# Kernel optimization log

Hardware: AMD Instinct MI355X
Metric: run time of the kernel (lower is better)

Reference implementation:

```python
import jax, jax.numpy as jnp
import numpy as np

N_XI = 512      # internal REN state dim
L = 128         # nonlinearity channels (sequential loop length)
N_STATES = 128  # plant state dim (w)
N_INPUTS = 64   # control input dim (u)
EPS = 0.001
STD = 0.1
BATCH = 32768


def _model_params(X, Y):
    """set_model_param(): derive constrained REN matrices from free params X, Y."""
    n, l = N_XI, L
    H = X.T @ X + EPS * jnp.eye(2 * n + l, dtype=X.dtype)
    H11 = H[:n, :n]
    H21 = H[n:n + l, :n]
    H22 = H[n:n + l, n:n + l]
    H31 = H[n + l:, :n]
    H32 = H[n + l:, n:n + l]
    H33 = H[n + l:, n + l:]
    Fm = H31                                 # (n_xi, n_xi)
    B1 = H32                                 # (n_xi, l)
    E = 0.5 * (H11 + H33 + Y - Y.T)          # (n_xi, n_xi)
    Lam = 0.5 * jnp.diag(H22)                # (l,) strictly positive
    D11 = -jnp.tril(H22, -1)                 # strictly lower triangular (l, l)
    C1 = -H21                                # (l, n_xi)
    return Fm, B1, E, Lam, D11, C1


def setup_inputs() -> dict:
    key = jax.random.key(0)
    ks = jax.random.split(key, 9)
    n, l = N_XI, L
    return {
        "t": 0,
        "w": jax.random.normal(ks[0], (BATCH, 1, N_STATES), jnp.float32),
        "xi": jax.random.normal(ks[1], (BATCH, 1, n), jnp.float32),
        "X": jax.random.normal(ks[2], (2 * n + l, 2 * n + l), jnp.float32) * STD,
        "Y": jax.random.normal(ks[3], (n, n), jnp.float32) * STD,
        "B2": jax.random.normal(ks[4], (n, N_STATES), jnp.float32) * STD,
        "C2": jax.random.normal(ks[5], (N_INPUTS, n), jnp.float32) * STD,
        "D21": jax.random.normal(ks[6], (N_INPUTS, l), jnp.float32) * STD,
        "D22": jax.random.normal(ks[7], (N_INPUTS, N_STATES), jnp.float32) * STD,
        "D12": jax.random.normal(ks[8], (l, N_STATES), jnp.float32) * STD,
    }


def reference(t, w, xi, X, Y, B2, C2, D21, D22, D12):
    Fm, B1, E, Lam, D11, C1 = _model_params(X, Y)
    w2 = w[:, 0, :]    # (B, num_states)
    xi2 = xi[:, 0, :]  # (B, n_xi)

    # Precompute the xi- and w-dependent parts of every row's pre-activation.
    pre = xi2 @ C1.T + w2 @ D12.T  # (B, l)

    eye = jnp.eye(L, dtype=pre.dtype)

    def step(eps, xs):
        # Sequential forward substitution: row i only reads eps[:, :i]
        # because D11 is strictly lower triangular.
        d_row, p_col, lam, e_row = xs
        v = p_col + eps @ d_row            # (B,)
        e = jnp.tanh(v / lam)
        return eps + e[:, None] * e_row[None, :], None

    eps0 = jnp.zeros_like(pre)
    epsilon, _ = jax.lax.scan(step, eps0, (D11, pre.T, Lam, eye))  # (B, l)

    E_xi = xi2 @ Fm.T + epsilon @ B1.T + w2 @ B2.T      # (B, n_xi)
    xi_ = E_xi @ jnp.linalg.inv(E).T                    # (B, n_xi)
    u = xi2 @ C2.T + epsilon @ D21.T + w2 @ D22.T       # (B, num_inputs)
    return u[:, None, :], xi_[:, None, :]
```

## Files before the change

kernel.cpp:

```cpp
#include <hip/hip_runtime.h>
#include <cstddef>

#define NXI   512
#define LL    128
#define NST   128
#define NU    64
#define BATCH 32768
#define TW    1152
#define EPSC  0.001f
#define KC    768
#define NC    576
#define NCP   640

typedef unsigned short u16;
typedef __attribute__((ext_vector_type(8))) short   short8;
typedef __attribute__((ext_vector_type(4))) short   short4v;
typedef __attribute__((ext_vector_type(4))) float   f32x4;

__device__ __forceinline__ u16 f2bf(float f) {
    unsigned u = __float_as_uint(f);
    u += 0x7FFFu + ((u >> 16) & 1u);
    return (u16)(u >> 16);
}

__global__ __launch_bounds__(256) void k_transpose(const float* __restrict__ X, u16* __restrict__ XT) {
    __shared__ float t[32][33];
    int tx = threadIdx.x & 31, ty = threadIdx.x >> 5;
    int bx = blockIdx.x, by = blockIdx.y;
    #pragma unroll
    for (int q = 0; q < 4; q++) {
        int r = ty + q * 8;
        t[r][tx] = X[(size_t)(by * 32 + r) * TW + bx * 32 + tx];
    }
    __syncthreads();
    #pragma unroll
    for (int q = 0; q < 4; q++) {
        int r = ty + q * 8;
        XT[(size_t)(bx * 32 + r) * TW + by * 32 + tx] = f2bf(t[tx][r]);
    }
}

__global__ __launch_bounds__(256) void k_build_Ac(const float* __restrict__ xi, const float* __restrict__ w,
                                                  u16* __restrict__ Ac) {
    size_t t = (size_t)blockIdx.x * 256 + threadIdx.x;
    int b = (int)(t / 80), ch = (int)(t % 80);
    const float* src;
    int col;
    if (ch < 64) { src = xi + (size_t)b * NXI + ch * 8;        col = ch * 8; }
    else         { src = w  + (size_t)b * NST + (ch - 64) * 8; col = 640 + (ch - 64) * 8; }
    f32x4 a = ((const f32x4*)src)[0], c = ((const f32x4*)src)[1];
    short8 o;
    o[0]=(short)f2bf(a[0]); o[1]=(short)f2bf(a[1]); o[2]=(short)f2bf(a[2]); o[3]=(short)f2bf(a[3]);
    o[4]=(short)f2bf(c[0]); o[5]=(short)f2bf(c[1]); o[6]=(short)f2bf(c[2]); o[7]=(short)f2bf(c[3]);
    *(short8*)(Ac + (size_t)b * KC + col) = o;
}

__global__ __launch_bounds__(256) void k_gemm2(const u16* __restrict__ A, int lda,
                                               const u16* __restrict__ W, int ldw,
                                               float* __restrict__ C0, int ldc0, int nsplit,
                                               float* __restrict__ C1, int ldc1,
                                               int K, int nbx, int ntrue, int swz) {
    __shared__ __align__(16) u16 As[128 * 32];
    __shared__ __align__(16) u16 Bs[128 * 32];
    int id = blockIdx.x;
    int bx, by;
    if (swz) {
        int j = id >> 3;
        int per = (int)(gridDim.x >> 3) / nbx;
        by = (id & 7) * per + j / nbx;
        bx = j - (j / nbx) * nbx;
    } else {
        by = id / nbx;
        bx = id - by * nbx;
    }
    const int tid = threadIdx.x;
    const int wave = tid >> 6, lane = tid & 63, quad = lane >> 4, l16 = lane & 15;
    const int bm0 = by * 128, bn0 = bx * 128;
    const int srow = tid >> 2, sch = (tid & 3) * 8;
    const u16* ga0 = A + (size_t)(bm0 + srow) * lda + sch;
    const u16* ga1 = ga0 + (size_t)64 * lda;
    const u16* gb0 = W + (size_t)(bn0 + srow) * ldw + sch;
    const u16* gb1 = gb0 + (size_t)64 * ldw;
    u16* la = As + wave * 512;
    u16* lb = Bs + wave * 512;
    const int mb = (wave >> 1) * 64, nb = (wave & 1) * 64;

    f32x4 acc[4][4];
    #pragma unroll
    for (int i = 0; i < 4; i++)
        #pragma unroll
        for (int j = 0; j < 4; j++) acc[i][j] = (f32x4){0.f, 0.f, 0.f, 0.f};

    for (int kt = 0; kt < K; kt += 32) {
        __syncthreads();
        __builtin_amdgcn_global_load_lds((void*)(ga0 + kt), (void*)la,          16, 0, 0);
        __builtin_amdgcn_global_load_lds((void*)(ga1 + kt), (void*)(la + 2048), 16, 0, 0);
        __builtin_amdgcn_global_load_lds((void*)(gb0 + kt), (void*)lb,          16, 0, 0);
        __builtin_amdgcn_global_load_lds((void*)(gb1 + kt), (void*)(lb + 2048), 16, 0, 0);
        __syncthreads();
        short8 af[4], bf[4];
        #pragma unroll
        for (int mt = 0; mt < 4; mt++) af[mt] = *(const short8*)&As[(mb + mt * 16 + l16) * 32 + quad * 8];
        #pragma unroll
        for (int nt = 0; nt < 4; nt++) bf[nt] = *(const short8*)&Bs[(nb + nt * 16 + l16) * 32 + quad * 8];
        #pragma unroll
        for (int mt = 0; mt < 4; mt++)
            #pragma unroll
            for (int nt = 0; nt < 4; nt++)
                acc[mt][nt] = __builtin_amdgcn_mfma_f32_16x16x32_bf16(af[mt], bf[nt], acc[mt][nt], 0, 0, 0);
    }
    #pragma unroll
    for (int mt = 0; mt < 4; mt++)
        #pragma unroll
        for (int nt = 0; nt < 4; nt++)
            #pragma unroll
            for (int r = 0; r < 4; r++) {
                int row = bm0 + mb + mt * 16 + quad * 4 + r;
                int col = bn0 + nb + nt * 16 + l16;
                if (col < ntrue) {
                    float v = acc[mt][nt][r];
                    if (col < nsplit) C0[(size_t)row * ldc0 + col] = v;
                    else              C1[(size_t)row * ldc1 + (col - nsplit)] = v;
                }
            }
}

__global__ __launch_bounds__(256) void k_derive(const float* __restrict__ Hm, const float* __restrict__ Y,
                                                const float* __restrict__ B2, const float* __restrict__ D12,
                                                float* __restrict__ Agj, float* __restrict__ D11,
                                                float* __restrict__ rlam, u16* __restrict__ W1) {
    int idx = blockIdx.x * 256 + threadIdx.x;
    const int n0 = 512 * 1280, n1 = 128 * 128, n2 = 128, n3 = 128 * KC;
    if (idx < n0) {
        int i = idx / 1280, j = idx % 1280;
        float val;
        if (j < 512) {
            val = 0.5f * (Hm[(size_t)i * TW + j] + Hm[(size_t)(640 + i) * TW + 640 + j]
                          + Y[(size_t)i * 512 + j] - Y[(size_t)j * 512 + i]);
            if (i == j) val += EPSC;
        } else if (j < 1024) {
            val = Hm[(size_t)(640 + i) * TW + (j - 512)];
        } else if (j < 1152) {
            val = Hm[(size_t)(640 + i) * TW + 512 + (j - 1024)];
        } else {
            val = B2[(size_t)i * NST + (j - 1152)];
        }
        Agj[idx] = val;
        return;
    }
    idx -= n0;
    if (idx < n1) {
        int i = idx >> 7, j = idx & 127;
        D11[idx] = (j < i) ? -Hm[(size_t)(512 + i) * TW + 512 + j] : 0.f;
        return;
    }
    idx -= n1;
    if (idx < n2) {
        rlam[idx] = 2.0f / (Hm[(size_t)(512 + idx) * TW + 512 + idx] + EPSC);
        return;
    }
    idx -= n2;
    if (idx < n3) {
        int i = idx / KC, c = idx % KC;
        float v;
        if (c < 512)      v = -Hm[(size_t)(512 + i) * TW + c];
        else if (c < 640) v = 0.f;
        else              v = D12[(size_t)i * NST + (c - 640)];
        W1[(size_t)i * KC + c] = f2bf(v);
    }
}

__device__ __forceinline__ void invert64(float* Cl, float* Sa, float* Sb, float* mcol,
                                         float* rp, float* __restrict__ invOut, int tid) {
    int r = tid >> 2, c = tid & 3;
    float a[16], b[16];
    #pragma unroll
    for (int q = 0; q < 4; q++) {
        f32x4 v = *(f32x4*)&Cl[r * 68 + c * 16 + q * 4];
        a[q*4+0]=v[0]; a[q*4+1]=v[1]; a[q*4+2]=v[2]; a[q*4+3]=v[3];
    }
    #pragma unroll
    for (int j = 0; j < 16; j++) b[j] = (c * 16 + j == r) ? 1.f : 0.f;

    #pragma unroll
    for (int k = 0; k < 64; k++) {
        const int kc = k >> 4, kl = k & 15;
        if (r == k) {
            #pragma unroll
            for (int q = 0; q < 4; q++) {
                *(f32x4*)&Sa[c * 16 + q * 4] = (f32x4){a[q*4], a[q*4+1], a[q*4+2], a[q*4+3]};
                *(f32x4*)&Sb[c * 16 + q * 4] = (f32x4){b[q*4], b[q*4+1], b[q*4+2], b[q*4+3]};
            }
        }
        if (c == kc) {
            mcol[r] = a[kl];
            if (r == k) rp[0] = 1.0f / a[kl];
        }
        __syncthreads();
        float m = (mcol[r] - ((r == k) ? 1.0f : 0.0f)) * rp[0];
        #pragma unroll
        for (int q = 0; q < 4; q++) {
            f32x4 sa = *(f32x4*)&Sa[c * 16 + q * 4];
            f32x4 sb = *(f32x4*)&Sb[c * 16 + q * 4];
            a[q*4+0] = fmaf(-m, sa[0], a[q*4+0]); a[q*4+1] = fmaf(-m, sa[1], a[q*4+1]);
            a[q*4+2] = fmaf(-m, sa[2], a[q*4+2]); a[q*4+3] = fmaf(-m, sa[3], a[q*4+3]);
            b[q*4+0] = fmaf(-m, sb[0], b[q*4+0]); b[q*4+1] = fmaf(-m, sb[1], b[q*4+1]);
            b[q*4+2] = fmaf(-m, sb[2], b[q*4+2]); b[q*4+3] = fmaf(-m, sb[3], b[q*4+3]);
        }
        __syncthreads();
    }
    #pragma unroll
    for (int q = 0; q < 4; q++)
        *(f32x4*)&invOut[r * 64 + c * 16 + q * 4] = (f32x4){b[q*4], b[q*4+1], b[q*4+2], b[q*4+3]};
}

__global__ __launch_bounds__(256) void k_diaginv0(const float* __restrict__ Agj, float* __restrict__ invD) {
    __shared__ __align__(16) float Cl[64 * 68];
    __shared__ float Sa[64], Sb[64], mcol[64], rp[1];
    int tid = threadIdx.x, r = tid >> 2, c4 = tid & 3;
    #pragma unroll
    for (int q = 0; q < 4; q++)
        *(f32x4*)&Cl[r * 68 + c4 * 16 + q * 4] = *(const f32x4*)(Agj + (size_t)r * 1280 + c4 * 16 + q * 4);
    __syncthreads();
    invert64(Cl, Sa, Sb, mcol, rp, invD, tid);
}

__global__ __launch_bounds__(256) void k_elim(float* __restrict__ Agj, float* __restrict__ invD, int k) {
    __shared__ __align__(16) float invDs[64 * 68];
    __shared__ __align__(16) float Ps[64 * 68];
    __shared__ __align__(16) float Ss[64 * 68];
    __shared__ __align__(16) float Ms[64 * 68];
    __shared__ float Sa[64], Sb[64], mcol[64], rp[1];
    int tid = threadIdx.x;
    int by = blockIdx.y, bx = blockIdx.x;
    int rb = by + (by >= k ? 1 : 0);
    int cb = k + 1 + bx;
    int lr = tid >> 2, lc = tid & 3;
    #pragma unroll
    for (int q = 0; q < 4; q++) {
        *(f32x4*)&invDs[lr * 68 + lc * 16 + q * 4] = *(const f32x4*)(invD + (size_t)k * 4096 + lr * 64 + lc * 16 + q * 4);
        *(f32x4*)&Ps[lr * 68 + lc * 16 + q * 4]    = *(const f32x4*)(Agj + (size_t)(k * 64 + lr) * 1280 + cb * 64 + lc * 16 + q * 4);
        *(f32x4*)&Ms[lr * 68 + lc * 16 + q * 4]    = *(const f32x4*)(Agj + (size_t)(rb * 64 + lr) * 1280 + k * 64 + lc * 16 + q * 4);
    }
    __syncthreads();
    int ty = tid >> 4, tx = tid & 15;
    f32x4 s[4];
    #pragma unroll
    for (int ri = 0; ri < 4; ri++) s[ri] = (f32x4){0.f, 0.f, 0.f, 0.f};
    for (int kk = 0; kk < 64; kk++) {
        f32x4 pv = *(f32x4*)&Ps[kk * 68 + tx * 4];
        #pragma unroll
        for (int ri = 0; ri < 4; ri++) s[ri] += pv * invDs[(ty * 4 + ri) * 68 + kk];
    }
    #pragma unroll
    for (int ri = 0; ri < 4; ri++) *(f32x4*)&Ss[(ty * 4 + ri) * 68 + tx * 4] = s[ri];
    __syncthreads();
    f32x4 accv[4];
    #pragma unroll
    for (int ri = 0; ri < 4; ri++)
        accv[ri] = *(const f32x4*)(Agj + (size_t)(rb * 64 + ty * 4 + ri) * 1280 + cb * 64 + tx * 4);
    for (int kk = 0; kk < 64; kk++) {
        f32x4 sv = *(f32x4*)&Ss[kk * 68 + tx * 4];
        #pragma unroll
        for (int ri = 0; ri < 4; ri++) accv[ri] -= sv * Ms[(ty * 4 + ri) * 68 + kk];
    }
    #pragma unroll
    for (int ri = 0; ri < 4; ri++)
        *(f32x4*)(Agj + (size_t)(rb * 64 + ty * 4 + ri) * 1280 + cb * 64 + tx * 4) = accv[ri];
    if (k < 7 && bx == 0 && by == k) {
        __syncthreads();
        #pragma unroll
        for (int ri = 0; ri < 4; ri++) *(f32x4*)&Ps[(ty * 4 + ri) * 68 + tx * 4] = accv[ri];
        __syncthreads();
        invert64(Ps, Sa, Sb, mcol, rp, invD + (size_t)(k + 1) * 4096, tid);
    }
}

__global__ __launch_bounds__(256) void k_finalize(const float* __restrict__ Agj, const float* __restrict__ invD,
                                                  const float* __restrict__ C2, const float* __restrict__ D21,
                                                  const float* __restrict__ D22, u16* __restrict__ Wc) {
    __shared__ __align__(16) float invDs[64 * 68];
    __shared__ __align__(16) float Ps[64 * 68];
    int tid = threadIdx.x, bx = blockIdx.x, by = blockIdx.y;
    int ty = tid >> 4, tx = tid & 15;
    if (by >= 8) {
        #pragma unroll
        for (int ri = 0; ri < 4; ri++) {
            int q = ty * 4 + ri;
            int row = 512 + (by - 8) * 64 + q;
            int cbase = bx * 64 + tx * 4;
            short4v o;
            if (by == 8) {
                f32x4 v;
                if (cbase < 512)      v = *(const f32x4*)(C2 + (size_t)q * 512 + cbase);
                else if (cbase < 640) v = *(const f32x4*)(D21 + (size_t)q * NST + (cbase - 512));
                else                  v = *(const f32x4*)(D22 + (size_t)q * NST + (cbase - 640));
                o[0]=(short)f2bf(v[0]); o[1]=(short)f2bf(v[1]); o[2]=(short)f2bf(v[2]); o[3]=(short)f2bf(v[3]);
            } else {
                o[0]=0; o[1]=0; o[2]=0; o[3]=0;
            }
            *(short4v*)(Wc + (size_t)row * KC + cbase) = o;
        }
        return;
    }
    int lr = tid >> 2, lc = tid & 3;
    #pragma unroll
    for (int q = 0; q < 4; q++) {
        *(f32x4*)&invDs[lr * 68 + lc * 16 + q * 4] = *(const f32x4*)(invD + (size_t)by * 4096 + lr * 64 + lc * 16 + q * 4);
        *(f32x4*)&Ps[lr * 68 + lc * 16 + q * 4]    = *(const f32x4*)(Agj + (size_t)(by * 64 + lr) * 1280 + 512 + bx * 64 + lc * 16 + q * 4);
    }
    __syncthreads();
    f32x4 s[4];
    #pragma unroll
    for (int ri = 0; ri < 4; ri++) s[ri] = (f32x4){0.f, 0.f, 0.f, 0.f};
    for (int kk = 0; kk < 64; kk++) {
        f32x4 pv = *(f32x4*)&Ps[kk * 68 + tx * 4];
        #pragma unroll
        for (int ri = 0; ri < 4; ri++) s[ri] += pv * invDs[(ty * 4 + ri) * 68 + kk];
    }
    #pragma unroll
    for (int ri = 0; ri < 4; ri++) {
        short4v o; o[0]=(short)f2bf(s[ri][0]); o[1]=(short)f2bf(s[ri][1]); o[2]=(short)f2bf(s[ri][2]); o[3]=(short)f2bf(s[ri][3]);
        *(short4v*)(Wc + (size_t)(by * 64 + ty * 4 + ri) * KC + bx * 64 + tx * 4) = o;
    }
}

__global__ __launch_bounds__(1024) void k_scan(const float* __restrict__ pre, const float* __restrict__ D11,
                                               const float* __restrict__ rlam, u16* __restrict__ Ac) {
    __shared__ __align__(16) float D11s[128 * 132];
    int tid = threadIdx.x;
    {
        int r = tid >> 3, c = (tid & 7) * 16;
        const f32x4* src = (const f32x4*)(D11 + (size_t)r * 128 + c);
        f32x4 v0 = src[0], v1 = src[1], v2 = src[2], v3 = src[3];
        f32x4* dst = (f32x4*)&D11s[r * 132 + c];
        dst[0] = v0; dst[1] = v1; dst[2] = v2; dst[3] = v3;
    }
    int lg = tid & 15;
    int row = blockIdx.x * 64 + (tid >> 4);
    int gbase = (tid & 63) & ~15;
    const float L2E2 = 2.885390082f;

    float corrv[8], a8[8];
    #pragma unroll
    for (int b = 0; b < 8; b++) {
        corrv[b] = pre[(size_t)row * 128 + b * 16 + lg];
        a8[b] = L2E2 * rlam[b * 16 + lg];
    }
    __syncthreads();

    #pragma unroll
    for (int b = 0; b < 8; b++) {
        f32x4 dblk[4];
        #pragma unroll
        for (int q = 0; q < 4; q++)
            dblk[q] = *(const f32x4*)&D11s[(b * 16 + lg) * 132 + b * 16 + q * 4];
        float v = corrv[b];
        float a = a8[b];
        float e16[16];
        float myeps = 0.f;
        #pragma unroll
        for (int t = 0; t < 16; t++) {
            float ex = __builtin_amdgcn_exp2f(a * v);
            float cand = 1.0f - 2.0f * __builtin_amdgcn_rcpf(ex + 1.0f);
            float e = __shfl(cand, gbase + t, 64);
            e16[t] = e;
            if (lg == t) myeps = e;
            v = fmaf(e, dblk[t >> 2][t & 3], v);
        }
        Ac[(size_t)row * KC + 512 + b * 16 + lg] = f2bf(myeps);
        #pragma unroll
        for (int bb = b + 1; bb < 8; bb++) {
            f32x4 dd[4];
            #pragma unroll
            for (int q = 0; q < 4; q++)
                dd[q] = *(const f32x4*)&D11s[(bb * 16 + lg) * 132 + b * 16 + q * 4];
            float acc = corrv[bb];
            #pragma unroll
            for (int t = 0; t < 16; t++)
                acc = fmaf(e16[t], dd[t >> 2][t & 3], acc);
            corrv[bb] = acc;
        }
    }
}

extern "C" void kernel_launch(void* const* d_in, const int* in_sizes, int n_in,
                              void* d_out, int out_size, void* d_ws, size_t ws_size,
                              hipStream_t stream) {
    const float* w_in  = (const float*)d_in[1];
    const float* xi_in = (const float*)d_in[2];
    const float* X   = (const float*)d_in[3];
    const float* Y   = (const float*)d_in[4];
    const float* B2  = (const float*)d_in[5];
    const float* C2  = (const float*)d_in[6];
    const float* D21 = (const float*)d_in[7];
    const float* D22 = (const float*)d_in[8];
    const float* D12 = (const float*)d_in[9];
    float* out_u  = (float*)d_out;
    float* out_xi = (float*)d_out + (size_t)BATCH * NU;

    char* base = (char*)d_ws;
    size_t off = 0;
    auto carve = [&](size_t bytes) -> void* {
        void* p = base + off;
        off += (bytes + 255) & ~(size_t)255;
        return p;
    };
    u16*   XT   = (u16*)  carve((size_t)TW * TW * 2);
    u16*   Ac   = (u16*)  carve((size_t)BATCH * KC * 2);
    float* Hm   = (float*)carve((size_t)TW * TW * 4);
    float* Agj  = (float*)carve((size_t)512 * 1280 * 4);
    float* invD = (float*)carve((size_t)8 * 64 * 64 * 4);
    u16*   Wc   = (u16*)  carve((size_t)NCP * KC * 2);
    u16*   W1   = (u16*)  carve((size_t)LL * KC * 2);
    float* pre  = (float*)carve((size_t)BATCH * LL * 4);
    float* D11  = (float*)carve((size_t)LL * LL * 4);
    float* rlam = (float*)carve((size_t)LL * 4);
    (void)ws_size; (void)in_sizes; (void)n_in; (void)out_size;

    k_transpose<<<dim3(36, 36), 256, 0, stream>>>(X, XT);
    k_build_Ac<<<BATCH * 80 / 256, 256, 0, stream>>>(xi_in, w_in, Ac);
    k_gemm2<<<81, 256, 0, stream>>>(XT, TW, XT, TW, Hm, TW, 1 << 30, nullptr, 0, TW, 9, TW, 0);
    k_derive<<<(512 * 1280 + 128 * 128 + 128 + 128 * KC + 255) / 256, 256, 0, stream>>>(
        Hm, Y, B2, D12, Agj, D11, rlam, W1);
    k_diaginv0<<<1, 256, 0, stream>>>(Agj, invD);
    for (int k = 0; k < 8; k++)
        k_elim<<<dim3(19 - k, 7), 256, 0, stream>>>(Agj, invD, k);
    k_finalize<<<dim3(12, 10), 256, 0, stream>>>(Agj, invD, C2, D21, D22, Wc);
    k_gemm2<<<256, 256, 0, stream>>>(Ac, KC, W1, KC, pre, LL, 1 << 30, nullptr, 0, KC, 1, LL, 1);
    k_scan<<<BATCH / 64, 1024, 0, stream>>>(pre, D11, rlam, Ac);
    k_gemm2<<<1280, 256, 0, stream>>>(Ac, KC, Wc, KC, out_xi, NXI, 512, out_u, NU, KC, 5, NC, 1);
}
```

Baseline: 527.1 us.

## Double-buffer GEMM LDS tiles, halve barriers in block inversion, merge setup kernels

The bf16 GEMM kernel now double-buffers its LDS tiles, issuing the next K-slice's global-to-LDS loads before computing on the current slice, with one barrier per iteration instead of two. The 64x64 Gauss-Jordan inversion ping-pongs its pivot-row scratch buffers so the trailing barrier per pivot step can be dropped. The transpose and input-packing kernels are merged into one launch to save a launch. These changes double GEMM LDS use, which may lower occupancy, and correctness depends on the async LDS loads being complete at the single barrier.

Result: no change. 522.3 us (-0.9%).

```diff
diff --git a/kernel.cpp b/kernel.cpp
--- a/kernel.cpp
+++ b/kernel.cpp
@@ -23,27 +23,29 @@
     return (u16)(u >> 16);
 }
 
-__global__ __launch_bounds__(256) void k_transpose(const float* __restrict__ X, u16* __restrict__ XT) {
+__global__ __launch_bounds__(256) void k_setup(const float* __restrict__ X, u16* __restrict__ XT,
+                                               const float* __restrict__ xi, const float* __restrict__ w,
+                                               u16* __restrict__ Ac) {
     __shared__ float t[32][33];
-    int tx = threadIdx.x & 31, ty = threadIdx.x >> 5;
-    int bx = blockIdx.x, by = blockIdx.y;
-    #pragma unroll
-    for (int q = 0; q < 4; q++) {
-        int r = ty + q * 8;
-        t[r][tx] = X[(size_t)(by * 32 + r) * TW + bx * 32 + tx];
-    }
-    __syncthreads();
-    #pragma unroll
-    for (int q = 0; q < 4; q++) {
-        int r = ty + q * 8;
-        XT[(size_t)(bx * 32 + r) * TW + by * 32 + tx] = f2bf(t[tx][r]);
-    }
-}
-
-__global__ __launch_bounds__(256) void k_build_Ac(const float* __restrict__ xi, const float* __restrict__ w,
-                                                  u16* __restrict__ Ac) {
-    size_t t = (size_t)blockIdx.x * 256 + threadIdx.x;
-    int b = (int)(t / 80), ch = (int)(t % 80);
+    int blk = blockIdx.x;
+    if (blk < 1296) {
+        int tx = threadIdx.x & 31, ty = threadIdx.x >> 5;
+        int bx = blk % 36, by = blk / 36;
+        #pragma unroll
+        for (int q = 0; q < 4; q++) {
+            int r = ty + q * 8;
+            t[r][tx] = X[(size_t)(by * 32 + r) * TW + bx * 32 + tx];
+        }
+        __syncthreads();
+        #pragma unroll
+        for (int q = 0; q < 4; q++) {
+            int r = ty + q * 8;
+            XT[(size_t)(bx * 32 + r) * TW + by * 32 + tx] = f2bf(t[tx][r]);
+        }
+        return;
+    }
+    size_t tt = (size_t)(blk - 1296) * 256 + threadIdx.x;
+    int b = (int)(tt / 80), ch = (int)(tt % 80);
     const float* src;
     int col;
     if (ch < 64) { src = xi + (size_t)b * NXI + ch * 8;        col = ch * 8; }
@@ -60,8 +62,8 @@
                                                float* __restrict__ C0, int ldc0, int nsplit,
                                                float* __restrict__ C1, int ldc1,
                                                int K, int nbx, int ntrue, int swz) {
-    __shared__ __align__(16) u16 As[128 * 32];
-    __shared__ __align__(16) u16 Bs[128 * 32];
+    __shared__ __align__(16) u16 As[2][128 * 32];
+    __shared__ __align__(16) u16 Bs[2][128 * 32];
     int id = blockIdx.x;
     int bx, by;
     if (swz) {
@@ -81,8 +83,7 @@
     const u16* ga1 = ga0 + (size_t)64 * lda;
     const u16* gb0 = W + (size_t)(bn0 + srow) * ldw + sch;
     const u16* gb1 = gb0 + (size_t)64 * ldw;
-    u16* la = As + wave * 512;
-    u16* lb = Bs + wave * 512;
+    const int lo = wave * 512;
     const int mb = (wave >> 1) * 64, nb = (wave & 1) * 64;
 
     f32x4 acc[4][4];
@@ -91,23 +92,36 @@
         #pragma unroll
         for (int j = 0; j < 4; j++) acc[i][j] = (f32x4){0.f, 0.f, 0.f, 0.f};
 
-    for (int kt = 0; kt < K; kt += 32) {
-        __syncthreads();
-        __builtin_amdgcn_global_load_lds((void*)(ga0 + kt), (void*)la,          16, 0, 0);
-        __builtin_amdgcn_global_load_lds((void*)(ga1 + kt), (void*)(la + 2048), 16, 0, 0);
-        __builtin_amdgcn_global_load_lds((void*)(gb0 + kt), (void*)lb,          16, 0, 0);
-        __builtin_amdgcn_global_load_lds((void*)(gb1 + kt), (void*)(lb + 2048), 16, 0, 0);
-        __syncthreads();
+    const int nk = K >> 5;
+    __builtin_amdgcn_global_load_lds((void*)(ga0), (void*)(As[0] + lo),        16, 0, 0);
+    __builtin_amdgcn_global_load_lds((void*)(ga1), (void*)(As[0] + lo + 2048), 16, 0, 0);
+    __builtin_amdgcn_global_load_lds((void*)(gb0), (void*)(Bs[0] + lo),        16, 0, 0);
+    __builtin_amdgcn_global_load_lds((void*)(gb1), (void*)(Bs[0] + lo + 2048), 16, 0, 0);
+    __syncthreads();
+    int cur = 0;
+    for (int t = 0; t < nk; ++t) {
+        if (t + 1 < nk) {
+            const int kt = (t + 1) << 5;
+            const int nx = cur ^ 1;
+            __builtin_amdgcn_global_load_lds((void*)(ga0 + kt), (void*)(As[nx] + lo),        16, 0, 0);
+            __builtin_amdgcn_global_load_lds((void*)(ga1 + kt), (void*)(As[nx] + lo + 2048), 16, 0, 0);
+            __builtin_amdgcn_global_load_lds((void*)(gb0 + kt), (void*)(Bs[nx] + lo),        16, 0, 0);
+            __builtin_amdgcn_global_load_lds((void*)(gb1 + kt), (void*)(Bs[nx] + lo + 2048), 16, 0, 0);
+        }
+        const u16* as = As[cur];
+        const u16* bs = Bs[cur];
         short8 af[4], bf[4];
         #pragma unroll
-        for (int mt = 0; mt < 4; mt++) af[mt] = *(const short8*)&As[(mb + mt * 16 + l16) * 32 + quad * 8];
-        #pragma unroll
-        for (int nt = 0; nt < 4; nt++) bf[nt] = *(const short8*)&Bs[(nb + nt * 16 + l16) * 32 + quad * 8];
+        for (int mt = 0; mt < 4; mt++) af[mt] = *(const short8*)&as[(mb + mt * 16 + l16) * 32 + quad * 8];
+        #pragma unroll
+        for (int nt = 0; nt < 4; nt++) bf[nt] = *(const short8*)&bs[(nb + nt * 16 + l16) * 32 + quad * 8];
         #pragma unroll
         for (int mt = 0; mt < 4; mt++)
             #pragma unroll
             for (int nt = 0; nt < 4; nt++)
                 acc[mt][nt] = __builtin_amdgcn_mfma_f32_16x16x32_bf16(af[mt], bf[nt], acc[mt][nt], 0, 0, 0);
+        __syncthreads();
+        cur ^= 1;
     }
     #pragma unroll
     for (int mt = 0; mt < 4; mt++)
@@ -184,30 +198,30 @@
 
     #pragma unroll
     for (int k = 0; k < 64; k++) {
+        const int p = (k & 1) << 6;
         const int kc = k >> 4, kl = k & 15;
         if (r == k) {
             #pragma unroll
             for (int q = 0; q < 4; q++) {
-                *(f32x4*)&Sa[c * 16 + q * 4] = (f32x4){a[q*4], a[q*4+1], a[q*4+2], a[q*4+3]};
-                *(f32x4*)&Sb[c * 16 + q * 4] = (f32x4){b[q*4], b[q*4+1], b[q*4+2], b[q*4+3]};
+                *(f32x4*)&Sa[p + c * 16 + q * 4] = (f32x4){a[q*4], a[q*4+1], a[q*4+2], a[q*4+3]};
+                *(f32x4*)&Sb[p + c * 16 + q * 4] = (f32x4){b[q*4], b[q*4+1], b[q*4+2], b[q*4+3]};
             }
         }
         if (c == kc) {
-            mcol[r] = a[kl];
-            if (r == k) rp[0] = 1.0f / a[kl];
+            mcol[p + r] = a[kl];
+            if (r == k) rp[k & 1] = 1.0f / a[kl];
         }
         __syncthreads();
-        float m = (mcol[r] - ((r == k) ? 1.0f : 0.0f)) * rp[0];
+        float m = (mcol[p + r] - ((r == k) ? 1.0f : 0.0f)) * rp[k & 1];
         #pragma unroll
         for (int q = 0; q < 4; q++) {
-            f32x4 sa = *(f32x4*)&Sa[c * 16 + q * 4];
-            f32x4 sb = *(f32x4*)&Sb[c * 16 + q * 4];
+            f32x4 sa = *(f32x4*)&Sa[p + c * 16 + q * 4];
+            f32x4 sb = *(f32x4*)&Sb[p + c * 16 + q * 4];
             a[q*4+0] = fmaf(-m, sa[0], a[q*4+0]); a[q*4+1] = fmaf(-m, sa[1], a[q*4+1]);
             a[q*4+2] = fmaf(-m, sa[2], a[q*4+2]); a[q*4+3] = fmaf(-m, sa[3], a[q*4+3]);
             b[q*4+0] = fmaf(-m, sb[0], b[q*4+0]); b[q*4+1] = fmaf(-m, sb[1], b[q*4+1]);
             b[q*4+2] = fmaf(-m, sb[2], b[q*4+2]); b[q*4+3] = fmaf(-m, sb[3], b[q*4+3]);
         }
-        __syncthreads();
     }
     #pragma unroll
     for (int q = 0; q < 4; q++)
@@ -216,7 +230,7 @@
 
 __global__ __launch_bounds__(256) void k_diaginv0(const float* __restrict__ Agj, float* __restrict__ invD) {
     __shared__ __align__(16) float Cl[64 * 68];
-    __shared__ float Sa[64], Sb[64], mcol[64], rp[1];
+    __shared__ float Sa[128], Sb[128], mcol[128], rp[2];
     int tid = threadIdx.x, r = tid >> 2, c4 = tid & 3;
     #pragma unroll
     for (int q = 0; q < 4; q++)
@@ -230,7 +244,7 @@
     __shared__ __align__(16) float Ps[64 * 68];
     __shared__ __align__(16) float Ss[64 * 68];
     __shared__ __align__(16) float Ms[64 * 68];
-    __shared__ float Sa[64], Sb[64], mcol[64], rp[1];
+    __shared__ float Sa[128], Sb[128], mcol[128], rp[2];
     int tid = threadIdx.x;
     int by = blockIdx.y, bx = blockIdx.x;
     int rb = by + (by >= k ? 1 : 0);
@@ -418,8 +432,7 @@
     float* rlam = (float*)carve((size_t)LL * 4);
     (void)ws_size; (void)in_sizes; (void)n_in; (void)out_size;
 
-    k_transpose<<<dim3(36, 36), 256, 0, stream>>>(X, XT);
-    k_build_Ac<<<BATCH * 80 / 256, 256, 0, stream>>>(xi_in, w_in, Ac);
+    k_setup<<<1296 + BATCH * 80 / 256, 256, 0, stream>>>(X, XT, xi_in, w_in, Ac);
     k_gemm2<<<81, 256, 0, stream>>>(XT, TW, XT, TW, Hm, TW, 1 << 30, nullptr, 0, TW, 9, TW, 0);
     k_derive<<<(512 * 1280 + 128 * 128 + 128 + 128 * KC + 255) / 256, 256, 0, stream>>>(
         Hm, Y, B2, D12, Agj, D11, rlam, W1);
```
